# Kernel tuning notes

Measured on AMD Instinct MI355X. Metric: run time of the kernel, lower is better.

The kernel has to match this reference:

```python
import jax, jax.numpy as jnp
import numpy as np

H = 512
L = 4
A = 16
EPS = 1e-5


def setup_inputs() -> dict:
    key = jax.random.key(0)
    ks = jax.random.split(key, 16)
    B, S = 64, 256
    scale = 0.02
    inp = {
        "hidden": jnp.zeros((B, H), jnp.float32),
        "x": jax.random.normal(ks[0], (B, S, H), jnp.float32),
        "dones": jax.random.randint(ks[1], (B, S), 0, 2).astype(bool),
        "avail_actions": jax.random.randint(ks[2], (B, S, A), 0, 2).astype(bool),
        # MLP stack: L layers of Linear(H,H) + LayerNorm
        "Wl": jax.random.normal(ks[3], (L, H, H), jnp.float32) * scale,
        "bl": jnp.zeros((L, H), jnp.float32),
        "ln_g": jnp.ones((L, H), jnp.float32),
        "ln_b": jnp.zeros((L, H), jnp.float32),
        # GRUCell(H, H): torch layout weight_ih [3H, H] (r, z, n order)
        "W_ih": jax.random.normal(ks[4], (3 * H, H), jnp.float32) * scale,
        "W_hh": jax.random.normal(ks[5], (3 * H, H), jnp.float32) * scale,
        "b_ih": jnp.zeros((3 * H,), jnp.float32),
        "b_hh": jnp.zeros((3 * H,), jnp.float32),
        # output head
        "Wq": jax.random.normal(ks[6], (A, H), jnp.float32) * scale,
        "bq": jnp.zeros((A,), jnp.float32),
    }
    return inp


def _layer_norm(x, g, b):
    mu = jnp.mean(x, axis=-1, keepdims=True)
    var = jnp.mean(jnp.square(x - mu), axis=-1, keepdims=True)
    return (x - mu) * jax.lax.rsqrt(var + EPS) * g + b


def _gru_scan(h0, x, dones, W_ih, W_hh, b_ih, b_hh):
    # Precompute input projections for all timesteps: [B, S, 3H]
    gi = jnp.einsum("bsh,gh->bsg", x, W_ih) + b_ih
    gi_t = jnp.swapaxes(gi, 0, 1)          # [S, B, 3H]
    dones_t = jnp.swapaxes(dones, 0, 1)    # [S, B]

    def step(h, inputs):
        gi_s, done_s = inputs
        h = jnp.where(done_s[:, None], 0.0, h)  # reset carry where done
        gh = h @ W_hh.T + b_hh
        i_r, i_z, i_n = jnp.split(gi_s, 3, axis=-1)
        h_r, h_z, h_n = jnp.split(gh, 3, axis=-1)
        r = jax.nn.sigmoid(i_r + h_r)
        z = jax.nn.sigmoid(i_z + h_z)
        n = jnp.tanh(i_n + r * h_n)
        h_new = (1.0 - z) * n + z * h
        return h_new, h_new

    h_final, outs = jax.lax.scan(step, h0, (gi_t, dones_t))
    return h_final, jnp.swapaxes(outs, 0, 1)  # [B, S, H]


def reference(hidden, x, dones, avail_actions, Wl, bl, ln_g, ln_b,
              W_ih, W_hh, b_ih, b_hh, Wq, bq):
    h = x
    for l in range(L):
        h = jnp.einsum("bsh,oh->bso", h, Wl[l]) + bl[l]
        h = jax.nn.relu(_layer_norm(h, ln_g[l], ln_b[l]))
    hidden_out, rnn_out = _gru_scan(hidden, h, dones, W_ih, W_hh, b_ih, b_hh)
    q = jnp.einsum("bsh,ah->bsa", rnn_out, Wq) + bq
    unavail = 1.0 - avail_actions.astype(q.dtype)
    q = q - unavail * 1e10
    return hidden_out, q
```

## Files before the change

### kernel.cpp

```cpp
#include <hip/hip_runtime.h>
#include <hip/hip_bf16.h>

typedef short short8 __attribute__((ext_vector_type(8)));
typedef float f32x4 __attribute__((ext_vector_type(4)));

#define H 512
#define BATCH 64
#define SEQ 256
#define NROWS 16384
#define NDOM 16
#define HSTCAP 12288

__device__ __forceinline__ float bf2f(unsigned short u) {
    union { unsigned int i; float f; } v;
    v.i = ((unsigned int)u) << 16;
    return v.f;
}
__device__ __forceinline__ unsigned short f2bf(float f) {
    union { float f; unsigned int i; } v;
    v.f = f;
    unsigned int lsb = (v.i >> 16) & 1u;
    v.i += 0x7fffu + lsb;
    return (unsigned short)(v.i >> 16);
}
__device__ __forceinline__ float sigm(float x) { return 1.f / (1.f + __expf(-x)); }
__device__ __forceinline__ float tanh_fast(float x) { return 2.f / (1.f + __expf(-2.f * x)) - 1.f; }

__global__ __launch_bounds__(256) void cvt_init(
    const float* __restrict__ Wl, const float* __restrict__ Wih,
    unsigned short* __restrict__ wlb, unsigned short* __restrict__ wihb,
    unsigned int* __restrict__ meta)
{
    long idx4 = (long)blockIdx.x * 256 + threadIdx.x;
    if (idx4 < 20480) meta[idx4] = 0u;
    long i = idx4 * 4;
    const long N1 = 1048576;
    const long N2 = N1 + 786432;
    const float* src; unsigned short* dst; long off;
    if (i < N1)      { src = Wl;  dst = wlb;  off = i; }
    else if (i < N2) { src = Wih; dst = wihb; off = i - N1; }
    else return;
    float4 v = *(const float4*)(src + off);
    ushort4 o;
    o.x = f2bf(v.x); o.y = f2bf(v.y); o.z = f2bf(v.z); o.w = f2bf(v.w);
    *(ushort4*)(dst + off) = o;
}

__global__ __launch_bounds__(256) void seg_build(
    const int* __restrict__ dones, int* __restrict__ lenArr,
    unsigned int* __restrict__ hist)
{
    __shared__ int d[256];
    const int b = blockIdx.x, s = threadIdx.x;
    d[s] = dones[b * 256 + s];
    __syncthreads();
    int len = 0;
    bool start = (s == 0) || (d[s] != 0);
    if (start) {
        len = 1;
        while (s + len < 256 && d[s + len] == 0) len++;
        atomicAdd(&hist[len], 1u);
    }
    lenArr[b * 256 + s] = len;
}

__global__ __launch_bounds__(256) void seg_offsets(
    const unsigned int* __restrict__ hist, int* __restrict__ Marr,
    unsigned int* __restrict__ offs, unsigned int* __restrict__ ssum)
{
    __shared__ unsigned int h[257];
    __shared__ int Msh[257];
    const int t = threadIdx.x;
    h[t] = hist[t];
    if (t == 0) h[256] = hist[256];
    __syncthreads();
    for (int tt = t; tt <= 256; tt += 256) {
        unsigned int m = 0;
        for (int L = tt + 1; L <= 256; ++L) m += h[L];
        Marr[tt] = (int)m;
        offs[tt] = m;
        Msh[tt] = (int)m;
    }
    __syncthreads();
    if (t == 0) {
        unsigned int acc = 0;
        for (int k = 0; k <= 256; ++k) { ssum[k] = acc; acc += (unsigned int)Msh[k]; }
    }
}

__global__ __launch_bounds__(256) void seg_scatter(
    const int* __restrict__ lenArr, unsigned int* __restrict__ offs,
    int* __restrict__ recs)
{
    const int b = blockIdx.x, s = threadIdx.x;
    int len = lenArr[b * 256 + s];
    if (len > 0) {
        unsigned int pos = atomicAdd(&offs[len], 1u);
        recs[pos] = (b << 16) | s;
    }
}

__global__ __launch_bounds__(256) void pmap_build(
    const int* __restrict__ recs, const int* __restrict__ Marr,
    const unsigned int* __restrict__ ssum, const int* __restrict__ lenArr,
    int* __restrict__ pmap)
{
    const int i = blockIdx.x * 256 + threadIdx.x;
    if (i >= Marr[0]) return;
    int rec = recs[i];
    int b = rec >> 16, st = rec & 0xffff;
    int len = lenArr[b * 256 + st];
    for (int t = 0; t < len; ++t) pmap[b * 256 + st + t] = (int)ssum[t] + i;
}

__global__ __launch_bounds__(256) void h_init(
    const int* __restrict__ recs, const int* __restrict__ Marr,
    const int* __restrict__ dones, const float* __restrict__ hidden,
    unsigned short* __restrict__ hst)
{
    const int w = threadIdx.x >> 6, lane = threadIdx.x & 63;
    const int i = blockIdx.x * 4 + w;
    const int nseg = Marr[0];
    const int c0 = lane * 8;
    unsigned short* dst = hst + (long)i * 512 + c0;
    if (i < nseg) {
        int rec = recs[i];
        int b = rec >> 16, st = rec & 0xffff;
        if (st == 0 && dones[b * 256] == 0) {
            float4 va = *(const float4*)(hidden + b * 512 + c0);
            float4 vb = *(const float4*)(hidden + b * 512 + c0 + 4);
            ushort4 o0 = {f2bf(va.x), f2bf(va.y), f2bf(va.z), f2bf(va.w)};
            ushort4 o1 = {f2bf(vb.x), f2bf(vb.y), f2bf(vb.z), f2bf(vb.w)};
            *(ushort4*)dst = o0; *(ushort4*)(dst + 4) = o1;
            return;
        }
    }
    ushort4 z4 = {0, 0, 0, 0};
    *(ushort4*)dst = z4; *(ushort4*)(dst + 4) = z4;
}

__global__ __launch_bounds__(256) void mlp_gi(
    const float* __restrict__ x,
    const unsigned short* __restrict__ wlb,
    const unsigned short* __restrict__ wihb,
    const float* __restrict__ bl,
    const float* __restrict__ lng,
    const float* __restrict__ lnb,
    const float* __restrict__ bih,
    const int* __restrict__ pmap,
    unsigned short* __restrict__ gi)
{
    __shared__ unsigned short ldsAct[32 * 512];
    __shared__ unsigned short ldsW[2][512 * 32];
    __shared__ float red[32 * 8];
    const int tid = threadIdx.x;
    const int lane = tid & 63;
    const int w = tid >> 6;
    const long m0 = (long)blockIdx.x * 32;
    const int l15 = lane & 15;
    const int l4 = lane >> 4;

    auto stage = [&](const unsigned short* W, int kt, int b) {
#pragma unroll
        for (int i = 0; i < 8; ++i) {
            int o = (i * 256 + tid) * 16;
            int row = o >> 6;
            int ch = (o & 63) >> 4;
            int sw = (row & 3) ^ ((row >> 2) & 3);
            long gcol = (long)kt * 64 + (long)((ch ^ sw) << 4);
            __builtin_amdgcn_global_load_lds(
                (const unsigned int*)((const char*)W + (long)row * 1024 + gcol),
                (unsigned int*)(ldsW[b] + (i * 256 + w * 64) * 8), 16, 0, 0);
        }
    };

#pragma unroll
    for (int it = 0; it < 8; ++it) {
        int ch = it * 256 + tid;
        int row = ch >> 6;
        int c = ch & 63;
        const float* xp = x + (m0 + row) * 512 + c * 8;
        float4 a = *(const float4*)xp;
        float4 b4 = *(const float4*)(xp + 4);
        short8 v;
        v[0] = (short)f2bf(a.x);  v[1] = (short)f2bf(a.y);
        v[2] = (short)f2bf(a.z);  v[3] = (short)f2bf(a.w);
        v[4] = (short)f2bf(b4.x); v[5] = (short)f2bf(b4.y);
        v[6] = (short)f2bf(b4.z); v[7] = (short)f2bf(b4.w);
        int byteo = (row * 1024 + c * 16) ^ ((row & 7) << 4);
        *(short8*)((char*)ldsAct + byteo) = v;
    }
    stage(wlb, 0, 0);
    __syncthreads();

    for (int u = 0; u < 7; ++u) {
        const unsigned short* W = (u < 4) ? (wlb + (long)u * 262144)
                                          : (wihb + (long)(u - 4) * 262144);
        const unsigned short* Wn = (u + 1 < 4) ? (wlb + (long)(u + 1) * 262144)
                                               : (wihb + (long)(u + 1 - 4) * 262144);
        f32x4 acc[2][8];
#pragma unroll
        for (int i = 0; i < 2; ++i)
#pragma unroll
            for (int jn = 0; jn < 8; ++jn) acc[i][jn] = (f32x4){0.f, 0.f, 0.f, 0.f};

        for (int kt = 0; kt < 16; ++kt) {
            const int cur = kt & 1;
            asm volatile("s_waitcnt vmcnt(0)" ::: "memory");
            __builtin_amdgcn_sched_barrier(0);
            __builtin_amdgcn_s_barrier();
            __builtin_amdgcn_sched_barrier(0);
            if (kt < 15)      stage(W,  kt + 1, cur ^ 1);
            else if (u < 6)   stage(Wn, 0,      cur ^ 1);
            __builtin_amdgcn_sched_barrier(0);

            short8 af[2], bfr[8];
#pragma unroll
            for (int i = 0; i < 2; ++i) {
                int arow = i * 16 + l15;
                int byteo = (arow * 1024 + kt * 64 + l4 * 16) ^ ((arow & 7) << 4);
                af[i] = *(const short8*)((const char*)ldsAct + byteo);
            }
#pragma unroll
            for (int jn = 0; jn < 8; ++jn) {
                int wrow = w * 128 + jn * 16 + l15;
                int sw = (wrow & 3) ^ ((wrow >> 2) & 3);
                int byteo = wrow * 64 + ((l4 ^ sw) << 4);
                bfr[jn] = *(const short8*)((const char*)(ldsW[cur]) + byteo);
            }
#pragma unroll
            for (int i = 0; i < 2; ++i)
#pragma unroll
                for (int jn = 0; jn < 8; ++jn)
                    acc[i][jn] = __builtin_amdgcn_mfma_f32_16x16x32_bf16(af[i], bfr[jn], acc[i][jn], 0, 0, 0);
        }

        if (u < 4) {
            float bz[8], gl[8], bb[8];
#pragma unroll
            for (int jn = 0; jn < 8; ++jn) {
                int n = w * 128 + jn * 16 + l15;
                bz[jn] = bl[u * 512 + n]; gl[jn] = lng[u * 512 + n]; bb[jn] = lnb[u * 512 + n];
            }
#pragma unroll
            for (int i = 0; i < 2; ++i)
#pragma unroll
                for (int jn = 0; jn < 8; ++jn)
#pragma unroll
                    for (int r = 0; r < 4; ++r) acc[i][jn][r] += bz[jn];

#pragma unroll
            for (int i = 0; i < 2; ++i) {
#pragma unroll
                for (int r = 0; r < 4; ++r) {
                    float sv = 0.f, qv = 0.f;
#pragma unroll
                    for (int jn = 0; jn < 8; ++jn) {
                        float v = acc[i][jn][r];
                        sv += v; qv += v * v;
                    }
                    sv += __shfl_xor(sv, 1); qv += __shfl_xor(qv, 1);
                    sv += __shfl_xor(sv, 2); qv += __shfl_xor(qv, 2);
                    sv += __shfl_xor(sv, 4); qv += __shfl_xor(qv, 4);
                    sv += __shfl_xor(sv, 8); qv += __shfl_xor(qv, 8);
                    if (l15 == 0) {
                        int row = i * 16 + l4 * 4 + r;
                        red[row * 8 + w * 2] = sv;
                        red[row * 8 + w * 2 + 1] = qv;
                    }
                }
            }
            __syncthreads();

#pragma unroll
            for (int i = 0; i < 2; ++i) {
#pragma unroll
                for (int r = 0; r < 4; ++r) {
                    int row = i * 16 + l4 * 4 + r;
                    float s_tot = red[row * 8 + 0] + red[row * 8 + 2] + red[row * 8 + 4] + red[row * 8 + 6];
                    float q_tot = red[row * 8 + 1] + red[row * 8 + 3] + red[row * 8 + 5] + red[row * 8 + 7];
                    float mu = s_tot * (1.f / 512.f);
                    float var = q_tot * (1.f / 512.f) - mu * mu;
                    float rs = rsqrtf(var + 1e-5f);
#pragma unroll
                    for (int jn = 0; jn < 8; ++jn) {
                        int col = w * 128 + jn * 16 + l15;
                        float v = fmaxf(0.f, (acc[i][jn][r] - mu) * rs * gl[jn] + bb[jn]);
                        int byteo = (row * 1024 + col * 2) ^ ((row & 7) << 4);
                        *(unsigned short*)((char*)ldsAct + byteo) = f2bf(v);
                    }
                }
            }
            __syncthreads();
        } else {
            const int nc = u - 4;
            __syncthreads();
#pragma unroll
            for (int jn = 0; jn < 8; ++jn) {
                int colg = nc * 512 + w * 128 + jn * 16 + l15;
                float bz = bih[colg];
#pragma unroll
                for (int i = 0; i < 2; ++i)
#pragma unroll
                    for (int r = 0; r < 4; ++r) {
                        int row = i * 16 + l4 * 4 + r;
                        int col = w * 128 + jn * 16 + l15;
                        int byteo = (row * 1024 + col * 2) ^ ((row & 7) << 4);
                        *(unsigned short*)((char*)(ldsW[1]) + byteo) = f2bf(acc[i][jn][r] + bz);
                    }
            }
            __syncthreads();
#pragma unroll
            for (int k = 0; k < 8; ++k) {
                int row = w * 8 + k;
                int pmr = pmap[m0 + row];
                int byteo = (row * 1024 + lane * 16) ^ ((row & 7) << 4);
                short8 v = *(const short8*)((const char*)(ldsW[1]) + byteo);
                *(short8*)(gi + (long)pmr * 1536 + nc * 512 + lane * 8) = v;
            }
            __syncthreads();
        }
    }
}

__device__ __forceinline__ void dbar(unsigned int* __restrict__ dm,
                                     int wg, unsigned int epoch)
{
    __syncthreads();
    const int tid = threadIdx.x;
    if (wg == 0) {
        if (tid == 0)
            __hip_atomic_store(&dm[0], epoch + 1u, __ATOMIC_RELAXED,
                               __HIP_MEMORY_SCOPE_AGENT);
        if (tid < 16) {
            while (__hip_atomic_load(&dm[tid * 32], __ATOMIC_RELAXED,
                                     __HIP_MEMORY_SCOPE_AGENT) <= epoch)
                __builtin_amdgcn_s_sleep(1);
        }
        if (tid == 0)
            __hip_atomic_store(&dm[512], epoch + 1u, __ATOMIC_RELAXED,
                               __HIP_MEMORY_SCOPE_AGENT);
    } else {
        if (tid == 0) {
            __hip_atomic_store(&dm[wg * 32], epoch + 1u, __ATOMIC_RELAXED,
                               __HIP_MEMORY_SCOPE_AGENT);
            while (__hip_atomic_load(&dm[512], __ATOMIC_RELAXED,
                                     __HIP_MEMORY_SCOPE_AGENT) <= epoch)
                __builtin_amdgcn_s_sleep(1);
        }
    }
    __syncthreads();
    __builtin_amdgcn_sched_barrier(0);
}

__global__ __launch_bounds__(256, 1) void gru_seg_scan(
    const unsigned short* __restrict__ gi,
    const float* __restrict__ Whh,
    const float* __restrict__ bhh,
    const int* __restrict__ Marr,
    const unsigned int* __restrict__ ssum,
    const int* __restrict__ recs,
    unsigned short* __restrict__ hstA,
    unsigned short* __restrict__ hstB,
    unsigned short* __restrict__ rnn,
    float* __restrict__ hid_out,
    unsigned int* __restrict__ meta)
{
    __shared__ unsigned short ldsW[96 * 512];
    __shared__ int sMarr[257];
    __shared__ unsigned int sssum[257];
    const int tid = threadIdx.x;
    const int lane = tid & 63;
    const int w = tid >> 6;
    const int jg = blockIdx.x >> 4;
    const int dom = blockIdx.x & 15;
    const int j0 = jg * 32;

    for (int e = tid; e < 96 * 512; e += 256) {
        int rrow = e >> 9;
        int col = e & 511;
        int gate = rrow >> 5;
        int jl = rrow & 31;
        float v = Whh[((long)(gate * 512 + j0 + jl)) * 512 + col];
        int byteo = (rrow * 1024 + col * 2) ^ ((rrow & 7) << 4);
        *(unsigned short*)((char*)ldsW + byteo) = f2bf(v);
    }
    for (int e = tid; e < 257; e += 256) { sMarr[e] = Marr[e]; sssum[e] = ssum[e]; }

    const int jl16 = lane & 15;
    float bhr[2], bhz[2], bhn[2];
#pragma unroll
    for (int jj = 0; jj < 2; ++jj) {
        int jc = j0 + jj * 16 + jl16;
        bhr[jj] = bhh[jc]; bhz[jj] = bhh[512 + jc]; bhn[jj] = bhh[1024 + jc];
    }
    const int rbase = w * 16 + (lane >> 4) * 4;
    const int arowl = w * 16 + jl16;
    const int kcol0 = (lane >> 4) * 8;
    unsigned int* dmeta = meta + 1024 * dom;
    __syncthreads();

    int crec[4], nrec[4];
    unsigned short cgr[4][2], cgz[4][2], cgn[4][2];
    unsigned short ngr[4][2], ngz[4][2], ngn[4][2];

    {
        const int Mt0 = sMarr[0];
        const long b0 = (long)sssum[0];
#pragma unroll
        for (int q = 0; q < 4; ++q) {
            int r = dom * 64 + rbase + q;
            if (r < Mt0) {
                crec[q] = recs[r];
#pragma unroll
                for (int jj = 0; jj < 2; ++jj) {
                    const unsigned short* gp = gi + (b0 + r) * 1536 + j0 + jj * 16 + jl16;
                    cgr[q][jj] = gp[0]; cgz[q][jj] = gp[512]; cgn[q][jj] = gp[1024];
                }
            } else crec[q] = -1;
        }
    }

    for (int t = 0; t < 256; ++t) {
        const int Mt = sMarr[t];
        if (Mt == 0) break;
        const int ntiles = (Mt + 63) >> 6;
        if (dom >= ntiles) break;
        const unsigned short* hsrc = (t & 1) ? hstB : hstA;
        unsigned short* hdst = (t & 1) ? hstA : hstB;
        const long base = (long)sssum[t];

        for (int tt = dom; tt < ntiles; tt += NDOM) {
            const int r0 = tt * 64;

            const unsigned short* arowp = hsrc + ((long)(r0 + arowl)) * 512 + kcol0;
            short8 af[16];
#pragma unroll
            for (int kk = 0; kk < 16; ++kk) {
                const unsigned short* ap = arowp + kk * 32;
                asm volatile("global_load_dwordx4 %0, %1, off sc0"
                             : "=v"(af[kk]) : "v"(ap));
            }
            unsigned int hu[4][2];
#pragma unroll
            for (int q = 0; q < 4; ++q)
#pragma unroll
                for (int jj = 0; jj < 2; ++jj) {
                    const unsigned short* hp = hsrc + (long)(r0 + rbase + q) * 512
                                             + j0 + jj * 16 + jl16;
                    asm volatile("global_load_ushort %0, %1, off sc0"
                                 : "=v"(hu[q][jj]) : "v"(hp));
                }
            asm volatile("s_waitcnt vmcnt(0)" ::: "memory");
            __builtin_amdgcn_sched_barrier(0);

            const bool instep = (tt + NDOM < ntiles);
            if (instep) {
#pragma unroll
                for (int q = 0; q < 4; ++q) {
                    int r = (tt + NDOM) * 64 + rbase + q;
                    if (r < Mt) {
                        nrec[q] = recs[r];
#pragma unroll
                        for (int jj = 0; jj < 2; ++jj) {
                            const unsigned short* gp = gi + (base + r) * 1536 + j0 + jj * 16 + jl16;
                            ngr[q][jj] = gp[0]; ngz[q][jj] = gp[512]; ngn[q][jj] = gp[1024];
                        }
                    } else nrec[q] = -1;
                }
            }

            f32x4 acch[3][2];
#pragma unroll
            for (int g = 0; g < 3; ++g)
#pragma unroll
                for (int jj = 0; jj < 2; ++jj) acch[g][jj] = (f32x4){0.f, 0.f, 0.f, 0.f};

#pragma unroll
            for (int kk = 0; kk < 16; ++kk) {
#pragma unroll
                for (int g = 0; g < 3; ++g)
#pragma unroll
                    for (int jj = 0; jj < 2; ++jj) {
                        int rrow = g * 32 + jj * 16 + jl16;
                        int bbyte = (rrow * 1024 + kk * 64 + ((lane >> 4) * 16)) ^ ((rrow & 7) << 4);
                        short8 bfrag = *(const short8*)((const char*)ldsW + bbyte);
                        acch[g][jj] = __builtin_amdgcn_mfma_f32_16x16x32_bf16(af[kk], bfrag, acch[g][jj], 0, 0, 0);
                    }
            }

#pragma unroll
            for (int q = 0; q < 4; ++q) {
                if (crec[q] >= 0) {
                    int r = r0 + rbase + q;
                    int b = crec[q] >> 16, st = crec[q] & 0xffff;
                    int s = st + t;
#pragma unroll
                    for (int jj = 0; jj < 2; ++jj) {
                        int jc = j0 + jj * 16 + jl16;
                        float heff = bf2f((unsigned short)hu[q][jj]);
                        float rgt = sigm(bf2f(cgr[q][jj]) + acch[0][jj][q] + bhr[jj]);
                        float zgt = sigm(bf2f(cgz[q][jj]) + acch[1][jj][q] + bhz[jj]);
                        float ngt = tanh_fast(bf2f(cgn[q][jj]) + rgt * (acch[2][jj][q] + bhn[jj]));
                        float hnew = (1.f - zgt) * ngt + zgt * heff;
                        unsigned short hb16 = f2bf(hnew);
                        hdst[(long)r * 512 + jc] = hb16;
                        rnn[((long)(b * 256 + s)) * 512 + jc] = hb16;
                        if (s == 255) hid_out[b * 512 + jc] = hnew;
                    }
                }
            }
            if (instep) {
#pragma unroll
                for (int q = 0; q < 4; ++q) {
                    crec[q] = nrec[q];
#pragma unroll
                    for (int jj = 0; jj < 2; ++jj) {
                        cgr[q][jj] = ngr[q][jj]; cgz[q][jj] = ngz[q][jj]; cgn[q][jj] = ngn[q][jj];
                    }
                }
            }
        }

        {
            const int Mt1 = sMarr[t + 1];
            if (Mt1 > 0 && dom < ((Mt1 + 63) >> 6)) {
                const long b1 = (long)sssum[t + 1];
#pragma unroll
                for (int q = 0; q < 4; ++q) {
                    int r = dom * 64 + rbase + q;
                    if (r < Mt1) {
                        crec[q] = recs[r];
#pragma unroll
                        for (int jj = 0; jj < 2; ++jj) {
                            const unsigned short* gp = gi + (b1 + r) * 1536 + j0 + jj * 16 + jl16;
                            cgr[q][jj] = gp[0]; cgz[q][jj] = gp[512]; cgn[q][jj] = gp[1024];
                        }
                    } else crec[q] = -1;
                }
            }
        }
        dbar(dmeta, jg, (unsigned int)t);
    }
}

__global__ __launch_bounds__(256) void qhead(
    const unsigned short* __restrict__ rnn, const float* __restrict__ Wq,
    const float* __restrict__ bq, const int* __restrict__ avail,
    float* __restrict__ qout)
{
    const int w = threadIdx.x >> 6;
    const int lane = threadIdx.x & 63;
    const long row = (long)blockIdx.x * 4 + w;
    const int a = lane & 15;
    const int kc = lane >> 4;
    const unsigned short* hr = rnn + row * H + kc * 128;
    const float* wr = Wq + a * H + kc * 128;
    float sum = 0.f;
#pragma unroll
    for (int i = 0; i < 128; i += 8) {
        short8 hv = *(const short8*)(hr + i);
        float4 wa = *(const float4*)(wr + i);
        float4 wb = *(const float4*)(wr + i + 4);
        sum += bf2f((unsigned short)hv[0]) * wa.x;
        sum += bf2f((unsigned short)hv[1]) * wa.y;
        sum += bf2f((unsigned short)hv[2]) * wa.z;
        sum += bf2f((unsigned short)hv[3]) * wa.w;
        sum += bf2f((unsigned short)hv[4]) * wb.x;
        sum += bf2f((unsigned short)hv[5]) * wb.y;
        sum += bf2f((unsigned short)hv[6]) * wb.z;
        sum += bf2f((unsigned short)hv[7]) * wb.w;
    }
    sum += __shfl_xor(sum, 16);
    sum += __shfl_xor(sum, 32);
    if (kc == 0) {
        float qv = sum + bq[a];
        int av = avail[row * 16 + a];
        if (av == 0) qv -= 1e10f;
        qout[row * 16 + a] = qv;
    }
}

extern "C" void kernel_launch(void* const* d_in, const int* in_sizes, int n_in,
                              void* d_out, int out_size, void* d_ws, size_t ws_size,
                              hipStream_t stream)
{
    const float* hidden = (const float*)d_in[0];
    const float* x      = (const float*)d_in[1];
    const int*   dones  = (const int*)d_in[2];
    const int*   avail  = (const int*)d_in[3];
    const float* Wl     = (const float*)d_in[4];
    const float* bl     = (const float*)d_in[5];
    const float* ln_g   = (const float*)d_in[6];
    const float* ln_b   = (const float*)d_in[7];
    const float* W_ih   = (const float*)d_in[8];
    const float* W_hh   = (const float*)d_in[9];
    const float* b_ih   = (const float*)d_in[10];
    const float* b_hh   = (const float*)d_in[11];
    const float* Wq     = (const float*)d_in[12];
    const float* bq     = (const float*)d_in[13];

    char* p = (char*)d_ws;
    unsigned short* gi   = (unsigned short*)p; p += (size_t)NROWS * 1536 * 2;
    unsigned short* rnn  = (unsigned short*)p; p += (size_t)NROWS * H * 2;
    unsigned short* hst0 = (unsigned short*)p; p += (size_t)HSTCAP * H * 2;
    unsigned short* hst1 = (unsigned short*)p; p += (size_t)HSTCAP * H * 2;
    unsigned short* wlb  = (unsigned short*)p; p += (size_t)4 * H * H * 2;
    unsigned short* wihb = (unsigned short*)p; p += (size_t)3 * H * H * 2;
    int* lenArr = (int*)p;          p += (size_t)NROWS * 4;
    int* recs   = (int*)p;          p += (size_t)NROWS * 4;
    int* pmap   = (int*)p;          p += (size_t)NROWS * 4;
    unsigned int* meta = (unsigned int*)p;  p += 20480 * 4;
    unsigned int* hist = meta + 16384;
    unsigned int* offs = meta + 16672;
    int* Marr = (int*)(meta + 16960);
    unsigned int* ssum = meta + 17248;

    cvt_init<<<1792, 256, 0, stream>>>(Wl, W_ih, wlb, wihb, meta);

    seg_build<<<64, 256, 0, stream>>>(dones, lenArr, hist);
    seg_offsets<<<1, 256, 0, stream>>>(hist, Marr, offs, ssum);
    seg_scatter<<<64, 256, 0, stream>>>(lenArr, offs, recs);
    pmap_build<<<64, 256, 0, stream>>>(recs, Marr, ssum, lenArr, pmap);

    h_init<<<HSTCAP / 4, 256, 0, stream>>>(recs, Marr, dones, hidden, hst0);

    mlp_gi<<<512, 256, 0, stream>>>(x, wlb, wihb, bl, ln_g, ln_b, b_ih, pmap, gi);

    gru_seg_scan<<<256, 256, 0, stream>>>(gi, W_hh, b_hh, Marr, ssum, recs,
                                          hst0, hst1, rnn, (float*)d_out, meta);

    qhead<<<4096, 256, 0, stream>>>(rnn, Wq, bq, avail, (float*)d_out + BATCH * H);
}
```

Measured before the change: 679.1 us.

## Single-buffer weight LDS in mlp_gi to fit two blocks per CU

Replaces the double-buffered weight staging in the MLP/input-projection kernel with a single LDS buffer loaded synchronously each k-step. This cuts LDS use from about 96KB to about 64KB per block, and with launch_bounds(256,2) it aims for two resident blocks per CU so one block's loads can overlap the other's compute. It also hoists the address computations out of the loop and raises wave priority around the MFMA block. The cost is that each block no longer prefetches, and there are two barriers per k-step.

Measured after the change: 613.9 us. -9.6%, faster.

```diff
diff --git a/kernel.cpp b/kernel.cpp
--- a/kernel.cpp
+++ b/kernel.cpp
@@ -139,7 +139,7 @@
     *(ushort4*)dst = z4; *(ushort4*)(dst + 4) = z4;
 }
 
-__global__ __launch_bounds__(256) void mlp_gi(
+__global__ __launch_bounds__(256, 2) void mlp_gi(
     const float* __restrict__ x,
     const unsigned short* __restrict__ wlb,
     const unsigned short* __restrict__ wihb,
@@ -151,7 +151,7 @@
     unsigned short* __restrict__ gi)
 {
     __shared__ unsigned short ldsAct[32 * 512];
-    __shared__ unsigned short ldsW[2][512 * 32];
+    __shared__ unsigned short ldsW[512 * 32];
     __shared__ float red[32 * 8];
     const int tid = threadIdx.x;
     const int lane = tid & 63;
@@ -160,19 +160,31 @@
     const int l15 = lane & 15;
     const int l4 = lane >> 4;
 
-    auto stage = [&](const unsigned short* W, int kt, int b) {
-#pragma unroll
-        for (int i = 0; i < 8; ++i) {
-            int o = (i * 256 + tid) * 16;
-            int row = o >> 6;
-            int ch = (o & 63) >> 4;
-            int sw = (row & 3) ^ ((row >> 2) & 3);
-            long gcol = (long)kt * 64 + (long)((ch ^ sw) << 4);
-            __builtin_amdgcn_global_load_lds(
-                (const unsigned int*)((const char*)W + (long)row * 1024 + gcol),
-                (unsigned int*)(ldsW[b] + (i * 256 + w * 64) * 8), 16, 0, 0);
-        }
-    };
+    int stSrc[8];
+    unsigned int* stDst[8];
+#pragma unroll
+    for (int i = 0; i < 8; ++i) {
+        int o = (i * 256 + tid) * 16;
+        int row = o >> 6;
+        int ch = (o & 63) >> 4;
+        int sw = (row & 3) ^ ((row >> 2) & 3);
+        stSrc[i] = row * 1024 + ((ch ^ sw) << 4);
+        stDst[i] = (unsigned int*)(ldsW + (i * 256 + w * 64) * 8);
+    }
+    int afBase[2], afSw[2];
+#pragma unroll
+    for (int i = 0; i < 2; ++i) {
+        int arow = i * 16 + l15;
+        afBase[i] = arow * 1024 + l4 * 16;
+        afSw[i] = (arow & 7) << 4;
+    }
+    int bfOff[8];
+#pragma unroll
+    for (int jn = 0; jn < 8; ++jn) {
+        int wrow = w * 128 + jn * 16 + l15;
+        int sw = (wrow & 3) ^ ((wrow >> 2) & 3);
+        bfOff[jn] = wrow * 64 + ((l4 ^ sw) << 4);
+    }
 
 #pragma unroll
     for (int it = 0; it < 8; ++it) {
@@ -190,14 +202,11 @@
         int byteo = (row * 1024 + c * 16) ^ ((row & 7) << 4);
         *(short8*)((char*)ldsAct + byteo) = v;
     }
-    stage(wlb, 0, 0);
     __syncthreads();
 
     for (int u = 0; u < 7; ++u) {
-        const unsigned short* W = (u < 4) ? (wlb + (long)u * 262144)
-                                          : (wihb + (long)(u - 4) * 262144);
-        const unsigned short* Wn = (u + 1 < 4) ? (wlb + (long)(u + 1) * 262144)
-                                               : (wihb + (long)(u + 1 - 4) * 262144);
+        const char* Wb = (u < 4) ? (const char*)(wlb + (long)u * 262144)
+                                 : (const char*)(wihb + (long)(u - 4) * 262144);
         f32x4 acc[2][8];
 #pragma unroll
         for (int i = 0; i < 2; ++i)
@@ -205,34 +214,28 @@
             for (int jn = 0; jn < 8; ++jn) acc[i][jn] = (f32x4){0.f, 0.f, 0.f, 0.f};
 
         for (int kt = 0; kt < 16; ++kt) {
-            const int cur = kt & 1;
-            asm volatile("s_waitcnt vmcnt(0)" ::: "memory");
-            __builtin_amdgcn_sched_barrier(0);
-            __builtin_amdgcn_s_barrier();
-            __builtin_amdgcn_sched_barrier(0);
-            if (kt < 15)      stage(W,  kt + 1, cur ^ 1);
-            else if (u < 6)   stage(Wn, 0,      cur ^ 1);
-            __builtin_amdgcn_sched_barrier(0);
+            const int ktb = kt * 64;
+            __syncthreads();
+#pragma unroll
+            for (int i = 0; i < 8; ++i)
+                __builtin_amdgcn_global_load_lds(
+                    (const unsigned int*)(Wb + stSrc[i] + ktb), stDst[i], 16, 0, 0);
+            __syncthreads();
 
             short8 af[2], bfr[8];
 #pragma unroll
-            for (int i = 0; i < 2; ++i) {
-                int arow = i * 16 + l15;
-                int byteo = (arow * 1024 + kt * 64 + l4 * 16) ^ ((arow & 7) << 4);
-                af[i] = *(const short8*)((const char*)ldsAct + byteo);
-            }
-#pragma unroll
-            for (int jn = 0; jn < 8; ++jn) {
-                int wrow = w * 128 + jn * 16 + l15;
-                int sw = (wrow & 3) ^ ((wrow >> 2) & 3);
-                int byteo = wrow * 64 + ((l4 ^ sw) << 4);
-                bfr[jn] = *(const short8*)((const char*)(ldsW[cur]) + byteo);
-            }
+            for (int i = 0; i < 2; ++i)
+                af[i] = *(const short8*)((const char*)ldsAct + ((afBase[i] + ktb) ^ afSw[i]));
+#pragma unroll
+            for (int jn = 0; jn < 8; ++jn)
+                bfr[jn] = *(const short8*)((const char*)ldsW + bfOff[jn]);
+            __builtin_amdgcn_s_setprio(1);
 #pragma unroll
             for (int i = 0; i < 2; ++i)
 #pragma unroll
                 for (int jn = 0; jn < 8; ++jn)
                     acc[i][jn] = __builtin_amdgcn_mfma_f32_16x16x32_bf16(af[i], bfr[jn], acc[i][jn], 0, 0, 0);
+            __builtin_amdgcn_s_setprio(0);
         }
 
         if (u < 4) {
@@ -306,7 +309,7 @@
                         int row = i * 16 + l4 * 4 + r;
                         int col = w * 128 + jn * 16 + l15;
                         int byteo = (row * 1024 + col * 2) ^ ((row & 7) << 4);
-                        *(unsigned short*)((char*)(ldsW[1]) + byteo) = f2bf(acc[i][jn][r] + bz);
+                        *(unsigned short*)((char*)ldsW + byteo) = f2bf(acc[i][jn][r] + bz);
                     }
             }
             __syncthreads();
@@ -315,10 +318,9 @@
                 int row = w * 8 + k;
                 int pmr = pmap[m0 + row];
                 int byteo = (row * 1024 + lane * 16) ^ ((row & 7) << 4);
-                short8 v = *(const short8*)((const char*)(ldsW[1]) + byteo);
+                short8 v = *(const short8*)((const char*)ldsW + byteo);
                 *(short8*)(gi + (long)pmr * 1536 + nc * 512 + lane * 8) = v;
             }
-            __syncthreads();
         }
     }
 }
```
